# Kernel optimization log

Measured on AMD Instinct MI355X. Metric: run time of the kernel, lower is better.

Reference implementation:

```python
import jax, jax.numpy as jnp
import numpy as np

B, U1, U2 = 4, 2048, 2048
C = 256      # in_feat_dim
F = 256      # feat_dim
M = 4        # num_modes
D = C // M   # attention_mode_dim = 64
ATTN_CLIP = 500.0
LN_EPS = 1e-12


def setup_inputs() -> dict:
    key = jax.random.key(0)
    ks = jax.random.split(key, 8)
    s = 0.02  # base_initializer_range
    inp = {
        "query_feat": jax.random.normal(ks[0], (B, U1, C), jnp.float32),
        "key_feat": jax.random.normal(ks[1], (B, U2, C), jnp.float32),
        "Wq": jax.random.normal(ks[2], (M * D, C), jnp.float32) * s,
        "bq": jnp.zeros((M * D,), jnp.float32),
    }
    # tie_qk_scheme='shared': key linear shares query weights
    inp["Wk"] = inp["Wq"]
    inp["bk"] = inp["bq"]
    inp["Wv"] = jax.random.normal(ks[3], (M * F, C), jnp.float32) * s  # first_linear, v_has_bias=False
    inp["W_mid"] = jax.random.normal(ks[4], (F, F), jnp.float32) * s   # MMSharedMid shared_linear
    inp["b_mid"] = jnp.zeros((F,), jnp.float32)
    inp["W_out"] = jax.random.normal(ks[5], (M, F, F), jnp.float32) * s  # grouped 1x1 conv, per mode
    inp["b_out"] = jnp.zeros((M, F), jnp.float32)
    inp["ln_g"] = jnp.ones((F,), jnp.float32)   # resout LayerNorm
    inp["ln_b"] = jnp.zeros((F,), jnp.float32)
    inp["W_score"] = jax.random.normal(ks[6], (1, F), jnp.float32) * s  # LearnedSoftAggregate
    inp["b_score"] = jnp.zeros((1,), jnp.float32)
    return inp


def _layer_norm(x, g, b):
    mu = jnp.mean(x, axis=-1, keepdims=True)
    var = jnp.var(x, axis=-1, keepdims=True)
    return (x - mu) * jax.lax.rsqrt(var + LN_EPS) * g + b


def reference(query_feat, key_feat, Wq, bq, Wk, bk, Wv, W_mid, b_mid,
              W_out, b_out, ln_g, ln_b, W_score, b_score):
    # --- tied-QK multi-mode attention ---
    q = (query_feat @ Wq.T + bq).reshape(B, U1, M, D)
    k = (key_feat @ Wk.T + bk).reshape(B, U2, M, D)
    scores = jnp.einsum('bimd,bjmd->bmij', q, k) / jnp.sqrt(jnp.float32(D))
    scores = jnp.clip(scores, -ATTN_CLIP, ATTN_CLIP)  # attn_clip
    probs = jax.nn.softmax(scores, axis=-1)           # [B, M, U1, U2]

    # --- ExpandedFeatTrans: value projection + fusion ---
    v = (key_feat @ Wv.T).reshape(B, U2, M, F)        # first_linear (no bias)
    fused = jnp.einsum('bmij,bjmf->bmif', probs, v)   # [B, M, U1, F]

    # MMSharedMid: shared linear over F + gelu (dropout = identity in eval)
    mid = jax.nn.gelu(fused @ W_mid.T + b_mid, approximate=False)

    # MMPrivateOutput: per-mode grouped 1x1 conv; NOTE the original code computes
    # x_comb = x + shortcut but then layer-norms x (shortcut dropped) - kept faithful.
    out = jnp.einsum('bmif,mgf->bmig', mid, W_out) + b_out[None, :, None, :]
    out = _layer_norm(out, ln_g, ln_b)                # [B, M, U1, F]

    # LearnedSoftAggregate over modes (group_dim=1, keepdim=False)
    mode_scores = out @ W_score.T + b_score           # [B, M, U1, 1]
    mode_probs = jax.nn.softmax(mode_scores, axis=1)
    return jnp.sum(out * mode_probs, axis=1)          # [B, U1, F]
```

## Files before the change

### kernel.cpp

```cpp
#include <hip/hip_runtime.h>

typedef __attribute__((ext_vector_type(8))) short short8;
typedef __attribute__((ext_vector_type(4))) float f32x4;
typedef __attribute__((ext_vector_type(16))) float f32x16;
typedef unsigned short u16t;
typedef unsigned int u32t;

#define MFMA16(a, b, c) __builtin_amdgcn_mfma_f32_16x16x32_bf16((a), (b), (c), 0, 0, 0)
#define MFMA32(a, b, c) __builtin_amdgcn_mfma_f32_32x32x16_bf16((a), (b), (c), 0, 0, 0)

__device__ __forceinline__ u16t f2bf(float f) {
  u32t u = __float_as_uint(f);
  u32t r = u + 0x7fffu + ((u >> 16) & 1u);
  return (u16t)(r >> 16);
}
__device__ __forceinline__ float bf2f(u16t b) {
  return __uint_as_float(((u32t)b) << 16);
}
__device__ __forceinline__ short8 pack8(float4 a0, float4 a1) {
  short8 r;
  r[0] = (short)f2bf(a0.x); r[1] = (short)f2bf(a0.y);
  r[2] = (short)f2bf(a0.z); r[3] = (short)f2bf(a0.w);
  r[4] = (short)f2bf(a1.x); r[5] = (short)f2bf(a1.y);
  r[6] = (short)f2bf(a1.z); r[7] = (short)f2bf(a1.w);
  return r;
}
__device__ __forceinline__ u32t packrhu(float a, float b) {
  u32t ua = __float_as_uint(a) + 0x8000u;
  u32t ub = __float_as_uint(b) + 0x8000u;
  return (ua >> 16) | (ub & 0xffff0000u);
}

__global__ __launch_bounds__(256) void cvt_kernel(
    const float* __restrict__ Wq, const float* __restrict__ Wv,
    const float* __restrict__ Wm, const float* __restrict__ Wo,
    u16t* __restrict__ WqB, u16t* __restrict__ WvB,
    u16t* __restrict__ WmB, u16t* __restrict__ WoB) {
  const int blk = blockIdx.x, tid = threadIdx.x;
  const float* src; u16t* dst; int base;
  if (blk < 64)       { src = Wq; dst = WqB; base = blk * 1024; }
  else if (blk < 320) { src = Wv; dst = WvB; base = (blk - 64) * 1024; }
  else if (blk < 384) { src = Wm; dst = WmB; base = (blk - 320) * 1024; }
  else                { src = Wo; dst = WoB; base = (blk - 384) * 1024; }
  int i = base + tid * 4;
  float4 v = *(const float4*)(src + i);
  ushort4 o;
  o.x = f2bf(v.x); o.y = f2bf(v.y); o.z = f2bf(v.z); o.w = f2bf(v.w);
  *(ushort4*)(dst + i) = o;
}

__global__ __launch_bounds__(256) void proj_kernel(
    const float* __restrict__ query, const float* __restrict__ key,
    const u16t* __restrict__ WqB, const u16t* __restrict__ WvB,
    const float* __restrict__ bq,
    u16t* __restrict__ QfB, u16t* __restrict__ KfB, u16t* __restrict__ VfB) {
  __shared__ __align__(16) u16t Cs[64 * 72];
  const int tid = threadIdx.x;
  const int w = tid >> 6, lane = tid & 63, quad = lane >> 4, l15 = lane & 15;
  const int l31 = lane & 31, h8 = (lane >> 5) * 8;
  const int wrow = (w >> 1) * 32, wcol = (w & 1) * 32;

  const int blk = blockIdx.x;
  const float* A; float ascale; int bx, nK, nV, kby0, vby0;
  u16t* out0;
  if (blk < 128) {
    A = query; ascale = 0.125f; bx = blk; nK = 4; nV = 0; kby0 = 0; vby0 = 0;
    out0 = QfB;
  } else {
    int kb = blk - 128;
    bx = kb & 127; int byg = kb >> 7;
    A = key; ascale = 1.0f; nK = 2; nV = 8; kby0 = byg * 2; vby0 = byg * 8;
    out0 = KfB;
  }
  const int rt = bx * 64;

  short8 af[8][2];
  {
    const float* arow0 = A + (size_t)(rt + wrow + l15) * 256;
    const float* arow1 = arow0 + 16 * 256;
#pragma unroll
    for (int ks = 0; ks < 8; ++ks) {
      const int kk = ks * 32 + quad * 8;
      float4 a00 = *(const float4*)(arow0 + kk);
      float4 a01 = *(const float4*)(arow0 + kk + 4);
      float4 a10 = *(const float4*)(arow1 + kk);
      float4 a11 = *(const float4*)(arow1 + kk + 4);
      a00.x *= ascale; a00.y *= ascale; a00.z *= ascale; a00.w *= ascale;
      a01.x *= ascale; a01.y *= ascale; a01.z *= ascale; a01.w *= ascale;
      a10.x *= ascale; a10.y *= ascale; a10.z *= ascale; a10.w *= ascale;
      a11.x *= ascale; a11.y *= ascale; a11.z *= ascale; a11.w *= ascale;
      af[ks][0] = pack8(a00, a01);
      af[ks][1] = pack8(a10, a11);
    }
  }

  const int ntiles = nK + nV;
#pragma unroll 1
  for (int tix = 0; tix < ntiles; ++tix) {
    const bool isK = tix < nK;
    const int by = isK ? (kby0 + tix) : (vby0 + (tix - nK));
    const u16t* W16 = isK ? WqB : WvB;
    u16t* outp = isK ? out0 : VfB;
    const int mode = isK ? 0 : 1;
    const int ct = by * 64;

    const f32x4 fz = {0.f, 0.f, 0.f, 0.f};
    f32x4 acc[2][2];
#pragma unroll
    for (int i = 0; i < 2; i++)
#pragma unroll
      for (int j = 0; j < 2; j++) acc[i][j] = fz;

    const u16t* wb0 = W16 + (size_t)(ct + wcol + l15) * 256;
#pragma unroll
    for (int ks = 0; ks < 8; ++ks) {
      const int kk = ks * 32 + quad * 8;
      short8 bw0 = *(const short8*)(wb0 + kk);
      short8 bw1 = *(const short8*)(wb0 + 16 * 256 + kk);
      acc[0][0] = MFMA16(af[ks][0], bw0, acc[0][0]);
      acc[0][1] = MFMA16(af[ks][0], bw1, acc[0][1]);
      acc[1][0] = MFMA16(af[ks][1], bw0, acc[1][0]);
      acc[1][1] = MFMA16(af[ks][1], bw1, acc[1][1]);
    }

    __syncthreads();
    if (mode == 0) {
#pragma unroll
      for (int i = 0; i < 2; i++) {
        int rl = wrow + i * 16 + quad * 4;
#pragma unroll
        for (int j = 0; j < 2; j++) {
          int cl = wcol + j * 16 + l15;
          float bv = bq[ct + cl] * ascale;
#pragma unroll
          for (int rg = 0; rg < 4; ++rg)
            Cs[(rl + rg) * 72 + cl] = f2bf(acc[i][j][rg] + bv);
        }
      }
    } else {
#pragma unroll
      for (int i = 0; i < 2; i++) {
        int rl = wrow + i * 16 + quad * 4;
#pragma unroll
        for (int j = 0; j < 2; j++) {
          int cl = wcol + j * 16 + l15;
          ushort4 pk;
          pk.x = f2bf(acc[i][j][0]);
          pk.y = f2bf(acc[i][j][1]);
          pk.z = f2bf(acc[i][j][2]);
          pk.w = f2bf(acc[i][j][3]);
          *(ushort4*)&Cs[cl * 72 + rl] = pk;
        }
      }
    }
    __syncthreads();
#pragma unroll
    for (int t2 = 0; t2 < 2; ++t2) {
      short8 frag = *(const short8*)&Cs[(t2 * 32 + l31) * 72 + w * 16 + h8];
      size_t base;
      if (mode == 0) {
        int b = rt >> 11, m = by;
        int it32 = ((rt & 2047) >> 5) + t2;
        base = (((size_t)(b * 4 + m) * 64 + it32) * 4 + w) * 512;
      } else {
        int b = rt >> 11, m = by >> 2;
        int fb = ((by & 3) << 1) + t2;
        int jt16 = ((rt & 2047) >> 4) + w;
        base = (((size_t)(b * 4 + m) * 8 + fb) * 128 + jt16) * 512;
      }
      *(short8*)(outp + base + lane * 8) = frag;
    }
  }
}

__global__ __launch_bounds__(256, 3) void attn_kernel(
    const u16t* __restrict__ Qf, const u16t* __restrict__ Kf,
    const u16t* __restrict__ Vf,
    const u16t* __restrict__ Wmid, const u16t* __restrict__ Wout,
    const float* __restrict__ b_mid, const float* __restrict__ b_out,
    const float* __restrict__ ln_g, const float* __restrict__ ln_b,
    const float* __restrict__ Wsc, const float* __restrict__ b_sc,
    u16t* __restrict__ out_ln, float* __restrict__ scoresWS) {
  __shared__ __align__(16) u16t smF[32 * 264];
  __shared__ __align__(16) u16t smP[2][32 * 132];
  __shared__ float smL[128];
  __shared__ float smR[128];
  __shared__ float smS[64];
  const int tid = threadIdx.x;
  const int w = tid >> 6, lane = tid & 63, quad = lane >> 4, l15 = lane & 15;
  const int l31 = lane & 31, h = lane >> 5;
  const int L = blockIdx.x;
  const int xcd = L & 7, slot = L >> 3;
  const int bm = xcd * 2 + (slot >> 6);
  const int it32 = slot & 63;
  const int m = bm & 3;
  const int q0 = it32 * 32;

  const size_t lane8 = (size_t)lane * 8;

  const u16t* qbase = Qf + ((size_t)(bm * 64 + it32) * 4) * 512 + lane8;
  short8 qf4[4];
#pragma unroll
  for (int ksd = 0; ksd < 4; ++ksd)
    qf4[ksd] = *(const short8*)(qbase + ksd * 512);

  const u16t* kbase = Kf + ((size_t)bm * 256) * 512 + lane8;
  const u16t* vbase = Vf + ((size_t)(bm * 8 + 2 * w) * 128) * 512 + lane8;

  f32x16 facc[2];
#pragma unroll
  for (int j = 0; j < 2; j++)
#pragma unroll
    for (int r = 0; r < 16; r++) facc[j][r] = 0.f;
  float lsum = 0.f;

  short8 kf4[4];
#pragma unroll
  for (int ksd = 0; ksd < 4; ++ksd)
    kf4[ksd] = *(const short8*)(kbase + (size_t)w * 2048 + ksd * 512);

  {
    f32x16 sacc;
#pragma unroll
    for (int r = 0; r < 16; r++) sacc[r] = 0.f;
#pragma unroll
    for (int ksd = 0; ksd < 4; ++ksd)
      sacc = MFMA32(kf4[ksd], qf4[ksd], sacc);
    float ls = 0.f;
#pragma unroll
    for (int tt = 0; tt < 8; ++tt) {
      const int jl = ((2 * tt) & 3) + 8 * ((2 * tt) >> 2) + 4 * h;
      float p0 = __expf(sacc[2 * tt]);
      float p1 = __expf(sacc[2 * tt + 1]);
      ls += p0 + p1;
      *(u32t*)&smP[0][l31 * 132 + w * 32 + jl] = packrhu(p0, p1);
    }
    lsum += ls;
  }
#pragma unroll
  for (int ksd = 0; ksd < 4; ++ksd)
    kf4[ksd] = *(const short8*)(kbase + (size_t)(4 + w) * 2048 + ksd * 512);
  __syncthreads();

#pragma unroll 1
  for (int t = 0; t < 16; ++t) {
    u16t* Pb = &smP[t & 1][0];
    u16t* Pn = &smP[(t + 1) & 1][0];

    short8 vf[16];
#pragma unroll
    for (int u = 0; u < 16; ++u)
      vf[u] = *(const short8*)(vbase + ((size_t)(u >> 3) * 128 + (t * 8 + (u & 7))) * 512);

    if (t < 15) {
      f32x16 sacc;
#pragma unroll
      for (int r = 0; r < 16; r++) sacc[r] = 0.f;
#pragma unroll
      for (int ksd = 0; ksd < 4; ++ksd)
        sacc = MFMA32(kf4[ksd], qf4[ksd], sacc);
      float ls = 0.f;
#pragma unroll
      for (int tt = 0; tt < 8; ++tt) {
        const int jl = ((2 * tt) & 3) + 8 * ((2 * tt) >> 2) + 4 * h;
        float p0 = __expf(sacc[2 * tt]);
        float p1 = __expf(sacc[2 * tt + 1]);
        ls += p0 + p1;
        *(u32t*)&Pn[l31 * 132 + w * 32 + jl] = packrhu(p0, p1);
      }
      lsum += ls;
    }
    if (t < 14) {
      const int jn = (t + 2) * 4 + w;
#pragma unroll
      for (int ksd = 0; ksd < 4; ++ksd)
        kf4[ksd] = *(const short8*)(kbase + (size_t)jn * 2048 + ksd * 512);
    }
#pragma unroll
    for (int jj = 0; jj < 4; ++jj) {
      short8 b0 = *(const short8*)&Pb[l31 * 132 + jj * 32 + h * 8];
      short8 b1 = *(const short8*)&Pb[l31 * 132 + jj * 32 + 16 + h * 8];
      facc[0] = MFMA32(vf[jj * 2], b0, facc[0]);
      facc[0] = MFMA32(vf[jj * 2 + 1], b1, facc[0]);
      facc[1] = MFMA32(vf[8 + jj * 2], b0, facc[1]);
      facc[1] = MFMA32(vf[8 + jj * 2 + 1], b1, facc[1]);
    }
    __syncthreads();
  }

  lsum += __shfl_xor(lsum, 32);
  if (h == 0) smL[w * 32 + l31] = lsum;
  __syncthreads();
  float inv = 1.f / (smL[l31] + smL[32 + l31] + smL[64 + l31] + smL[96 + l31]);

#pragma unroll
  for (int fb = 0; fb < 2; ++fb) {
#pragma unroll
    for (int g = 0; g < 4; ++g) {
      int fbase = w * 64 + fb * 32 + 8 * g + 4 * h;
      ushort4 pk4;
      pk4.x = f2bf(facc[fb][4 * g + 0] * inv);
      pk4.y = f2bf(facc[fb][4 * g + 1] * inv);
      pk4.z = f2bf(facc[fb][4 * g + 2] * inv);
      pk4.w = f2bf(facc[fb][4 * g + 3] * inv);
      *(ushort4*)&smF[l31 * 264 + fbase] = pk4;
    }
  }
  __syncthreads();

  const int rgrp = w >> 1, ch = w & 1;
  const int rowq = rgrp * 16 + quad * 4;
  const f32x4 fz4 = {0.f, 0.f, 0.f, 0.f};

  f32x4 macc[8];
#pragma unroll
  for (int i = 0; i < 8; i++) macc[i] = fz4;
  for (int kc = 0; kc < 8; ++kc) {
    short8 af = *(const short8*)&smF[(rgrp * 16 + l15) * 264 + kc * 32 + quad * 8];
#pragma unroll
    for (int nb = 0; nb < 8; ++nb) {
      short8 bw = *(const short8*)(Wmid + (size_t)(ch * 128 + nb * 16 + l15) * 256 + kc * 32 + quad * 8);
      macc[nb] = MFMA16(af, bw, macc[nb]);
    }
  }
#pragma unroll
  for (int nb = 0; nb < 8; ++nb) {
    int c = ch * 128 + nb * 16 + l15;
    float bmv = b_mid[c];
#pragma unroll
    for (int rg = 0; rg < 4; ++rg) {
      float x = macc[nb][rg] + bmv;
      macc[nb][rg] = 0.5f * x * (1.f + erff(x * 0.70710678118654752f));
    }
  }
  __syncthreads();
#pragma unroll
  for (int nb = 0; nb < 8; ++nb)
#pragma unroll
    for (int rg = 0; rg < 4; ++rg)
      smF[(rowq + rg) * 264 + ch * 128 + nb * 16 + l15] = f2bf(macc[nb][rg]);
  __syncthreads();

  const u16t* Wo = Wout + (size_t)m * 65536;
  f32x4 oacc[8];
#pragma unroll
  for (int i = 0; i < 8; i++) oacc[i] = fz4;
  for (int kc = 0; kc < 8; ++kc) {
    short8 af = *(const short8*)&smF[(rgrp * 16 + l15) * 264 + kc * 32 + quad * 8];
#pragma unroll
    for (int nb = 0; nb < 8; ++nb) {
      short8 bw = *(const short8*)(Wo + (size_t)(ch * 128 + nb * 16 + l15) * 256 + kc * 32 + quad * 8);
      oacc[nb] = MFMA16(af, bw, oacc[nb]);
    }
  }

  float sum[4] = {0, 0, 0, 0}, sq[4] = {0, 0, 0, 0};
#pragma unroll
  for (int nb = 0; nb < 8; ++nb) {
    int c = ch * 128 + nb * 16 + l15;
    float bo = b_out[m * 256 + c];
#pragma unroll
    for (int rg = 0; rg < 4; ++rg) {
      float x = oacc[nb][rg] + bo;
      oacc[nb][rg] = x;
      sum[rg] += x;
      sq[rg] += x * x;
    }
  }
#pragma unroll
  for (int rg = 0; rg < 4; ++rg) {
    float s = sum[rg], s2 = sq[rg];
    s += __shfl_xor(s, 1); s += __shfl_xor(s, 2); s += __shfl_xor(s, 4); s += __shfl_xor(s, 8);
    s2 += __shfl_xor(s2, 1); s2 += __shfl_xor(s2, 2); s2 += __shfl_xor(s2, 4); s2 += __shfl_xor(s2, 8);
    if (l15 == 0) {
      smR[(rowq + rg) + 32 * ch] = s;
      smR[64 + (rowq + rg) + 32 * ch] = s2;
    }
  }
  __syncthreads();
  float mu[4], rstd[4];
#pragma unroll
  for (int rg = 0; rg < 4; ++rg) {
    int r = rowq + rg;
    float s = smR[r] + smR[r + 32];
    float s2 = smR[64 + r] + smR[64 + r + 32];
    float mean = s * (1.f / 256.f);
    float var = s2 * (1.f / 256.f) - mean * mean;
    mu[rg] = mean;
    rstd[rg] = rsqrtf(var + 1e-12f);
  }

  float scp[4] = {0, 0, 0, 0};
#pragma unroll
  for (int nb = 0; nb < 8; ++nb) {
    int c = ch * 128 + nb * 16 + l15;
    float g = ln_g[c], bb2 = ln_b[c], wsv = Wsc[c];
#pragma unroll
    for (int rg = 0; rg < 4; ++rg) {
      float xn = (oacc[nb][rg] - mu[rg]) * rstd[rg] * g + bb2;
      out_ln[((size_t)bm * 2048 + (q0 + rowq + rg)) * 256 + c] = f2bf(xn);
      scp[rg] += xn * wsv;
    }
  }
#pragma unroll
  for (int rg = 0; rg < 4; ++rg) {
    float s = scp[rg];
    s += __shfl_xor(s, 1); s += __shfl_xor(s, 2); s += __shfl_xor(s, 4); s += __shfl_xor(s, 8);
    if (l15 == 0) smS[(rowq + rg) + 32 * ch] = s;
  }
  __syncthreads();
  if (ch == 0 && l15 == 0) {
#pragma unroll
    for (int rg = 0; rg < 4; ++rg) {
      int r = rowq + rg;
      scoresWS[bm * 2048 + q0 + r] = smS[r] + smS[r + 32] + b_sc[0];
    }
  }
}

__global__ __launch_bounds__(256) void agg_kernel(
    const u16t* __restrict__ out_ln, const float* __restrict__ scoresWS,
    float* __restrict__ out) {
  const int row = blockIdx.x;
  const int c = threadIdx.x;
  const int b = row >> 11, i = row & 2047;
  float s0 = scoresWS[(b * 4 + 0) * 2048 + i];
  float s1 = scoresWS[(b * 4 + 1) * 2048 + i];
  float s2 = scoresWS[(b * 4 + 2) * 2048 + i];
  float s3 = scoresWS[(b * 4 + 3) * 2048 + i];
  float mx = fmaxf(fmaxf(s0, s1), fmaxf(s2, s3));
  float e0 = __expf(s0 - mx), e1 = __expf(s1 - mx), e2 = __expf(s2 - mx), e3 = __expf(s3 - mx);
  float inv = 1.f / (e0 + e1 + e2 + e3);
  float acc = e0 * inv * bf2f(out_ln[((size_t)(b * 4 + 0) * 2048 + i) * 256 + c]) +
              e1 * inv * bf2f(out_ln[((size_t)(b * 4 + 1) * 2048 + i) * 256 + c]) +
              e2 * inv * bf2f(out_ln[((size_t)(b * 4 + 2) * 2048 + i) * 256 + c]) +
              e3 * inv * bf2f(out_ln[((size_t)(b * 4 + 3) * 2048 + i) * 256 + c]);
  out[(size_t)row * 256 + c] = acc;
}

extern "C" void kernel_launch(void* const* d_in, const int* in_sizes, int n_in,
                              void* d_out, int out_size, void* d_ws, size_t ws_size,
                              hipStream_t stream) {
  (void)in_sizes; (void)n_in; (void)out_size; (void)ws_size;
  const float* query = (const float*)d_in[0];
  const float* key   = (const float*)d_in[1];
  const float* Wq    = (const float*)d_in[2];
  const float* bq    = (const float*)d_in[3];
  const float* Wv    = (const float*)d_in[6];
  const float* Wm    = (const float*)d_in[7];
  const float* bmid  = (const float*)d_in[8];
  const float* Wo    = (const float*)d_in[9];
  const float* bo    = (const float*)d_in[10];
  const float* lng   = (const float*)d_in[11];
  const float* lnb   = (const float*)d_in[12];
  const float* Wsc   = (const float*)d_in[13];
  const float* bsc   = (const float*)d_in[14];

  char* p = (char*)d_ws;
  u16t* QfB = (u16t*)p; p += (size_t)2097152 * 2;
  u16t* KfB = (u16t*)p; p += (size_t)2097152 * 2;
  u16t* VfB = (u16t*)p; p += (size_t)8388608 * 2;
  u16t* WmB = (u16t*)p; p += (size_t)65536 * 2;
  u16t* WoB = (u16t*)p; p += (size_t)262144 * 2;
  u16t* WqB = (u16t*)p; p += (size_t)65536 * 2;
  u16t* WvB = (u16t*)p; p += (size_t)262144 * 2;
  u16t* outLn = (u16t*)p; p += (size_t)8388608 * 2;
  float* scWS = (float*)p; p += (size_t)32768 * 4;

  cvt_kernel<<<640, 256, 0, stream>>>(Wq, Wv, Wm, Wo, WqB, WvB, WmB, WoB);

  proj_kernel<<<384, 256, 0, stream>>>(query, key, WqB, WvB, bq,
                                       QfB, KfB, VfB);

  attn_kernel<<<1024, 256, 0, stream>>>(QfB, KfB, VfB, WmB, WoB,
                                        bmid, bo, lng, lnb, Wsc, bsc,
                                        outLn, scWS);

  agg_kernel<<<8192, 256, 0, stream>>>(outLn, scWS, (float*)d_out);
}
```

Measured before the change: 270.8 us.

## Fold weight conversion into projection, split per-tile grid, raise attention occupancy

The separate weight-conversion kernel is removed. The projection kernel now reads fp32 Wq/Wv directly and converts them to bf16 in registers, while extra blocks convert W_mid/W_out. The projection grid is expanded to one block per 64x64 output tile with XCD-aware block mapping, replacing the old per-block loop over tiles. In the attention kernel the P double buffer and F staging share one LDS array, V fragments are loaded per inner step instead of 16 at once, and launch bounds are raised to 4 blocks per SU to cut register and LDS pressure; this exposes more V load latency and repeats the A-fragment load across tiles.

```diff
diff --git a/kernel.cpp b/kernel.cpp
--- a/kernel.cpp
+++ b/kernel.cpp
@@ -31,48 +31,45 @@
   return (ua >> 16) | (ub & 0xffff0000u);
 }
 
-__global__ __launch_bounds__(256) void cvt_kernel(
-    const float* __restrict__ Wq, const float* __restrict__ Wv,
-    const float* __restrict__ Wm, const float* __restrict__ Wo,
-    u16t* __restrict__ WqB, u16t* __restrict__ WvB,
-    u16t* __restrict__ WmB, u16t* __restrict__ WoB) {
-  const int blk = blockIdx.x, tid = threadIdx.x;
-  const float* src; u16t* dst; int base;
-  if (blk < 64)       { src = Wq; dst = WqB; base = blk * 1024; }
-  else if (blk < 320) { src = Wv; dst = WvB; base = (blk - 64) * 1024; }
-  else if (blk < 384) { src = Wm; dst = WmB; base = (blk - 320) * 1024; }
-  else                { src = Wo; dst = WoB; base = (blk - 384) * 1024; }
-  int i = base + tid * 4;
-  float4 v = *(const float4*)(src + i);
-  ushort4 o;
-  o.x = f2bf(v.x); o.y = f2bf(v.y); o.z = f2bf(v.z); o.w = f2bf(v.w);
-  *(ushort4*)(dst + i) = o;
-}
-
 __global__ __launch_bounds__(256) void proj_kernel(
     const float* __restrict__ query, const float* __restrict__ key,
-    const u16t* __restrict__ WqB, const u16t* __restrict__ WvB,
+    const float* __restrict__ Wq, const float* __restrict__ Wv,
     const float* __restrict__ bq,
+    const float* __restrict__ Wm, const float* __restrict__ Wo,
+    u16t* __restrict__ WmB, u16t* __restrict__ WoB,
     u16t* __restrict__ QfB, u16t* __restrict__ KfB, u16t* __restrict__ VfB) {
+  const int tid = threadIdx.x;
+  const int blk = blockIdx.x;
+
+  if (blk >= 3072) {
+    int cv = blk - 3072;
+    const float* src; u16t* dst; int base;
+    if (cv < 64) { src = Wm; dst = WmB; base = cv * 1024; }
+    else         { src = Wo; dst = WoB; base = (cv - 64) * 1024; }
+    int i = base + tid * 4;
+    float4 v = *(const float4*)(src + i);
+    ushort4 o2;
+    o2.x = f2bf(v.x); o2.y = f2bf(v.y); o2.z = f2bf(v.z); o2.w = f2bf(v.w);
+    *(ushort4*)(dst + i) = o2;
+    return;
+  }
+
   __shared__ __align__(16) u16t Cs[64 * 72];
-  const int tid = threadIdx.x;
   const int w = tid >> 6, lane = tid & 63, quad = lane >> 4, l15 = lane & 15;
   const int l31 = lane & 31, h8 = (lane >> 5) * 8;
   const int wrow = (w >> 1) * 32, wcol = (w & 1) * 32;
 
-  const int blk = blockIdx.x;
-  const float* A; float ascale; int bx, nK, nV, kby0, vby0;
-  u16t* out0;
-  if (blk < 128) {
-    A = query; ascale = 0.125f; bx = blk; nK = 4; nV = 0; kby0 = 0; vby0 = 0;
-    out0 = QfB;
-  } else {
-    int kb = blk - 128;
-    bx = kb & 127; int byg = kb >> 7;
-    A = key; ascale = 1.0f; nK = 2; nV = 8; kby0 = byg * 2; vby0 = byg * 8;
-    out0 = KfB;
-  }
+  const int xcd = blk & 7, o = blk >> 3;
+  const int tix = o % 24, bxl = o / 24;
+  const int bx = bxl * 8 + xcd;
   const int rt = bx * 64;
+
+  const float* A; const float* W; float ascale; u16t* outp; int mode, by;
+  bool hasbias;
+  if (tix < 4)      { A = query; W = Wq; ascale = 0.125f; outp = QfB; mode = 0; by = tix;     hasbias = true; }
+  else if (tix < 8) { A = key;   W = Wq; ascale = 1.0f;   outp = KfB; mode = 0; by = tix - 4; hasbias = true; }
+  else              { A = key;   W = Wv; ascale = 1.0f;   outp = VfB; mode = 1; by = tix - 8; hasbias = false; }
+  const int ct = by * 64;
 
   short8 af[8][2];
   {
@@ -94,86 +91,79 @@
     }
   }
 
-  const int ntiles = nK + nV;
-#pragma unroll 1
-  for (int tix = 0; tix < ntiles; ++tix) {
-    const bool isK = tix < nK;
-    const int by = isK ? (kby0 + tix) : (vby0 + (tix - nK));
-    const u16t* W16 = isK ? WqB : WvB;
-    u16t* outp = isK ? out0 : VfB;
-    const int mode = isK ? 0 : 1;
-    const int ct = by * 64;
-
-    const f32x4 fz = {0.f, 0.f, 0.f, 0.f};
-    f32x4 acc[2][2];
-#pragma unroll
-    for (int i = 0; i < 2; i++)
-#pragma unroll
-      for (int j = 0; j < 2; j++) acc[i][j] = fz;
-
-    const u16t* wb0 = W16 + (size_t)(ct + wcol + l15) * 256;
-#pragma unroll
-    for (int ks = 0; ks < 8; ++ks) {
-      const int kk = ks * 32 + quad * 8;
-      short8 bw0 = *(const short8*)(wb0 + kk);
-      short8 bw1 = *(const short8*)(wb0 + 16 * 256 + kk);
-      acc[0][0] = MFMA16(af[ks][0], bw0, acc[0][0]);
-      acc[0][1] = MFMA16(af[ks][0], bw1, acc[0][1]);
-      acc[1][0] = MFMA16(af[ks][1], bw0, acc[1][0]);
-      acc[1][1] = MFMA16(af[ks][1], bw1, acc[1][1]);
-    }
-
-    __syncthreads();
+  const f32x4 fz = {0.f, 0.f, 0.f, 0.f};
+  f32x4 acc[2][2];
+#pragma unroll
+  for (int i = 0; i < 2; i++)
+#pragma unroll
+    for (int j = 0; j < 2; j++) acc[i][j] = fz;
+
+  const float* wrow0 = W + (size_t)(ct + wcol + l15) * 256;
+  const float* wrow1 = wrow0 + 16 * 256;
+#pragma unroll 4
+  for (int ks = 0; ks < 8; ++ks) {
+    const int kk = ks * 32 + quad * 8;
+    float4 w00 = *(const float4*)(wrow0 + kk);
+    float4 w01 = *(const float4*)(wrow0 + kk + 4);
+    float4 w10 = *(const float4*)(wrow1 + kk);
+    float4 w11 = *(const float4*)(wrow1 + kk + 4);
+    short8 bw0 = pack8(w00, w01);
+    short8 bw1 = pack8(w10, w11);
+    acc[0][0] = MFMA16(af[ks][0], bw0, acc[0][0]);
+    acc[0][1] = MFMA16(af[ks][0], bw1, acc[0][1]);
+    acc[1][0] = MFMA16(af[ks][1], bw0, acc[1][0]);
+    acc[1][1] = MFMA16(af[ks][1], bw1, acc[1][1]);
+  }
+
+  if (mode == 0) {
+#pragma unroll
+    for (int i = 0; i < 2; i++) {
+      int rl = wrow + i * 16 + quad * 4;
+#pragma unroll
+      for (int j = 0; j < 2; j++) {
+        int cl = wcol + j * 16 + l15;
+        float bv = hasbias ? bq[ct + cl] * ascale : 0.f;
+#pragma unroll
+        for (int rg = 0; rg < 4; ++rg)
+          Cs[(rl + rg) * 72 + cl] = f2bf(acc[i][j][rg] + bv);
+      }
+    }
+  } else {
+#pragma unroll
+    for (int i = 0; i < 2; i++) {
+      int rl = wrow + i * 16 + quad * 4;
+#pragma unroll
+      for (int j = 0; j < 2; j++) {
+        int cl = wcol + j * 16 + l15;
+        ushort4 pk;
+        pk.x = f2bf(acc[i][j][0]);
+        pk.y = f2bf(acc[i][j][1]);
+        pk.z = f2bf(acc[i][j][2]);
+        pk.w = f2bf(acc[i][j][3]);
+        *(ushort4*)&Cs[cl * 72 + rl] = pk;
+      }
+    }
+  }
+  __syncthreads();
+#pragma unroll
+  for (int t2 = 0; t2 < 2; ++t2) {
+    short8 frag = *(const short8*)&Cs[(t2 * 32 + l31) * 72 + w * 16 + h8];
+    size_t base;
     if (mode == 0) {
-#pragma unroll
-      for (int i = 0; i < 2; i++) {
-        int rl = wrow + i * 16 + quad * 4;
-#pragma unroll
-        for (int j = 0; j < 2; j++) {
-          int cl = wcol + j * 16 + l15;
-          float bv = bq[ct + cl] * ascale;
-#pragma unroll
-          for (int rg = 0; rg < 4; ++rg)
-            Cs[(rl + rg) * 72 + cl] = f2bf(acc[i][j][rg] + bv);
-        }
-      }
+      int b = rt >> 11, m = by;
+      int it32 = ((rt & 2047) >> 5) + t2;
+      base = (((size_t)(b * 4 + m) * 64 + it32) * 4 + w) * 512;
     } else {
-#pragma unroll
-      for (int i = 0; i < 2; i++) {
-        int rl = wrow + i * 16 + quad * 4;
-#pragma unroll
-        for (int j = 0; j < 2; j++) {
-          int cl = wcol + j * 16 + l15;
-          ushort4 pk;
-          pk.x = f2bf(acc[i][j][0]);
-          pk.y = f2bf(acc[i][j][1]);
-          pk.z = f2bf(acc[i][j][2]);
-          pk.w = f2bf(acc[i][j][3]);
-          *(ushort4*)&Cs[cl * 72 + rl] = pk;
-        }
-      }
-    }
-    __syncthreads();
-#pragma unroll
-    for (int t2 = 0; t2 < 2; ++t2) {
-      short8 frag = *(const short8*)&Cs[(t2 * 32 + l31) * 72 + w * 16 + h8];
-      size_t base;
-      if (mode == 0) {
-        int b = rt >> 11, m = by;
-        int it32 = ((rt & 2047) >> 5) + t2;
-        base = (((size_t)(b * 4 + m) * 64 + it32) * 4 + w) * 512;
-      } else {
-        int b = rt >> 11, m = by >> 2;
-        int fb = ((by & 3) << 1) + t2;
-        int jt16 = ((rt & 2047) >> 4) + w;
-        base = (((size_t)(b * 4 + m) * 8 + fb) * 128 + jt16) * 512;
-      }
-      *(short8*)(outp + base + lane * 8) = frag;
-    }
-  }
-}
-
-__global__ __launch_bounds__(256, 3) void attn_kernel(
+      int b = rt >> 11, m = by >> 2;
+      int fb = ((by & 3) << 1) + t2;
+      int jt16 = ((rt & 2047) >> 4) + w;
+      base = (((size_t)(b * 4 + m) * 8 + fb) * 128 + jt16) * 512;
+    }
+    *(short8*)(outp + base + lane * 8) = frag;
+  }
+}
+
+__global__ __launch_bounds__(256, 4) void attn_kernel(
     const u16t* __restrict__ Qf, const u16t* __restrict__ Kf,
     const u16t* __restrict__ Vf,
     const u16t* __restrict__ Wmid, const u16t* __restrict__ Wout,
@@ -181,8 +171,7 @@
     const float* __restrict__ ln_g, const float* __restrict__ ln_b,
     const float* __restrict__ Wsc, const float* __restrict__ b_sc,
     u16t* __restrict__ out_ln, float* __restrict__ scoresWS) {
-  __shared__ __align__(16) u16t smF[32 * 264];
-  __shared__ __align__(16) u16t smP[2][32 * 132];
+  __shared__ __align__(16) u16t smU[8448];
   __shared__ float smL[128];
   __shared__ float smR[128];
   __shared__ float smS[64];
@@ -233,7 +222,7 @@
       float p0 = __expf(sacc[2 * tt]);
       float p1 = __expf(sacc[2 * tt + 1]);
       ls += p0 + p1;
-      *(u32t*)&smP[0][l31 * 132 + w * 32 + jl] = packrhu(p0, p1);
+      *(u32t*)&smU[l31 * 132 + w * 32 + jl] = packrhu(p0, p1);
     }
     lsum += ls;
   }
@@ -244,13 +233,8 @@
 
 #pragma unroll 1
   for (int t = 0; t < 16; ++t) {
-    u16t* Pb = &smP[t & 1][0];
-    u16t* Pn = &smP[(t + 1) & 1][0];
-
-    short8 vf[16];
-#pragma unroll
-    for (int u = 0; u < 16; ++u)
-      vf[u] = *(const short8*)(vbase + ((size_t)(u >> 3) * 128 + (t * 8 + (u & 7))) * 512);
+    u16t* Pb = (t & 1) ? smU + 4224 : smU;
+    u16t* Pn = (t & 1) ? smU : smU + 4224;
 
     if (t < 15) {
       f32x16 sacc;
@@ -278,12 +262,20 @@
     }
 #pragma unroll
     for (int jj = 0; jj < 4; ++jj) {
-      short8 b0 = *(const short8*)&Pb[l31 * 132 + jj * 32 + h * 8];
-      short8 b1 = *(const short8*)&Pb[l31 * 132 + jj * 32 + 16 + h * 8];
-      facc[0] = MFMA32(vf[jj * 2], b0, facc[0]);
-      facc[0] = MFMA32(vf[jj * 2 + 1], b1, facc[0]);
-      facc[1] = MFMA32(vf[8 + jj * 2], b0, facc[1]);
-      facc[1] = MFMA32(vf[8 + jj * 2 + 1], b1, facc[1]);
+      short8 vf[2][2];
+#pragma unroll
+      for (int fb = 0; fb < 2; ++fb)
+#pragma unroll
+        for (int ks2 = 0; ks2 < 2; ++ks2)
+          vf[fb][ks2] = *(const short8*)(vbase + ((size_t)fb * 128 + (t * 8 + jj * 2 + ks2)) * 512);
+      short8 bbL[2];
+#pragma unroll
+      for (int ks2 = 0; ks2 < 2; ++ks2)
+        bbL[ks2] = *(const short8*)&Pb[l31 * 132 + jj * 32 + ks2 * 16 + h * 8];
+      facc[0] = MFMA32(vf[0][0], bbL[0], facc[0]);
+      facc[0] = MFMA32(vf[0][1], bbL[1], facc[0]);
+      facc[1] = MFMA32(vf[1][0], bbL[0], facc[1]);
+      facc[1] = MFMA32(vf[1][1], bbL[1], facc[1]);
     }
     __syncthreads();
   }
@@ -293,6 +285,7 @@
   __syncthreads();
   float inv = 1.f / (smL[l31] + smL[32 + l31] + smL[64 + l31] + smL[96 + l31]);
 
+  u16t* const smF = smU;
 #pragma unroll
   for (int fb = 0; fb < 2; ++fb) {
 #pragma unroll
@@ -462,15 +455,11 @@
   u16t* VfB = (u16t*)p; p += (size_t)8388608 * 2;
   u16t* WmB = (u16t*)p; p += (size_t)65536 * 2;
   u16t* WoB = (u16t*)p; p += (size_t)262144 * 2;
-  u16t* WqB = (u16t*)p; p += (size_t)65536 * 2;
-  u16t* WvB = (u16t*)p; p += (size_t)262144 * 2;
   u16t* outLn = (u16t*)p; p += (size_t)8388608 * 2;
   float* scWS = (float*)p; p += (size_t)32768 * 4;
 
-  cvt_kernel<<<640, 256, 0, stream>>>(Wq, Wv, Wm, Wo, WqB, WvB, WmB, WoB);
-
-  proj_kernel<<<384, 256, 0, stream>>>(query, key, WqB, WvB, bq,
-                                       QfB, KfB, VfB);
+  proj_kernel<<<3392, 256, 0, stream>>>(query, key, Wq, Wv, bq, Wm, Wo,
+                                        WmB, WoB, QfB, KfB, VfB);
 
   attn_kernel<<<1024, 256, 0, stream>>>(QfB, KfB, VfB, WmB, WoB,
                                         bmid, bo, lng, lnb, Wsc, bsc,
```

Measured after the change: 337.6 us. 1.25x slower.
